# Kernel tuning notes

Hardware: AMD Instinct MI355X
Metric: run time of the kernel (lower is better)

## Reference

```python
import jax, jax.numpy as jnp
import numpy as np

RES = 128          # occupancy grid resolution per axis
S = 320            # fixed number of marching steps per ray
STEP = 0.01        # render_step_size
NEAR = 0.0         # near_plane
ALPHA_THRE = 0.01  # alpha_sample_thre


def setup_inputs() -> dict:
    key = jax.random.key(0)
    k1, k2, k3 = jax.random.split(key, 3)
    N = 16384
    # ray origins inside the scene aabb [-1,1]^3
    origins = (jax.random.uniform(k1, (N, 3), dtype=jnp.float32) - 0.5)
    d = jax.random.normal(k2, (N, 3), dtype=jnp.float32)
    directions = d / jnp.linalg.norm(d, axis=-1, keepdims=True)
    # per-cell densities of the occupancy grid (occupancy_grid.occs)
    occs = jax.random.uniform(k3, (RES, RES, RES), dtype=jnp.float32)
    aabb = jnp.array([[-1.0, -1.0, -1.0], [1.0, 1.0, 1.0]], dtype=jnp.float32)
    return {"origins": origins, "directions": directions, "occs": occs, "aabb": aabb}


def _ray_aabb(o, d, aabb):
    # robust slab intersection; returns (t_min, t_max) per ray
    safe_d = jnp.where(jnp.abs(d) < 1e-10, 1e-10, d)
    inv = 1.0 / safe_d
    t0 = (aabb[0] - o) * inv
    t1 = (aabb[1] - o) * inv
    tmin = jnp.max(jnp.minimum(t0, t1), axis=-1)
    tmax = jnp.min(jnp.maximum(t0, t1), axis=-1)
    return jnp.maximum(tmin, NEAR), tmax


def reference(origins, directions, occs, aabb):
    N = origins.shape[0]
    tmin, tmax = _ray_aabb(origins, directions, aabb)           # [N]
    i = jnp.arange(S, dtype=origins.dtype)
    t_starts = tmin[:, None] + i[None, :] * STEP                # [N,S]
    t_ends = t_starts + STEP
    t_mid = 0.5 * (t_starts + t_ends)
    # sample midpoints along each ray: [N,S,3]
    pos = origins[:, None, :] + directions[:, None, :] * t_mid[..., None]
    # occupancy-grid query (nerfacc.grid._query style)
    u = (pos - aabb[0]) / (aabb[1] - aabb[0])                   # [N,S,3] in [0,1)
    idx = jnp.clip(jnp.floor(u * RES).astype(jnp.int32), 0, RES - 1)
    occ = occs[idx[..., 0], idx[..., 1], idx[..., 2]]           # [N,S] gather
    inside = jnp.all((u >= 0.0) & (u < 1.0), axis=-1)           # [N,S]
    # alpha = 1 - exp(-render_step_size * density), as in update_binary_grid
    alpha = 1.0 - jnp.exp(-occ * STEP)
    mask = inside & (t_ends <= tmax[:, None]) & (alpha > ALPHA_THRE) \
           & (tmax[:, None] > tmin[:, None])                    # [N,S]
    ray_indices = jnp.broadcast_to(
        jnp.arange(N, dtype=jnp.int32)[:, None], mask.shape)
    maskf = mask.astype(pos.dtype)
    positions = pos * maskf[..., None]                          # compacted-by-mask
    return (positions,
            t_starts * maskf,
            t_ends * maskf,
            jnp.where(mask, ray_indices, -1),
            mask)
```

## Files before the change

### kernel.cpp

```cpp
#include <hip/hip_runtime.h>

#define RES 128
#define NSTEPS 320
#define STEP 0.01f
#define ALPHA_THRE 0.01f

__global__ __launch_bounds__(NSTEPS) void nerfacc_sampler_kernel(
    const float* __restrict__ origins,
    const float* __restrict__ dirs,
    const float* __restrict__ occs,
    const float* __restrict__ aabb,
    float* __restrict__ out,
    int N)
{
    const int r = blockIdx.x;
    const int j = threadIdx.x;

    const float ox = origins[r * 3 + 0];
    const float oy = origins[r * 3 + 1];
    const float oz = origins[r * 3 + 2];
    const float dx = dirs[r * 3 + 0];
    const float dy = dirs[r * 3 + 1];
    const float dz = dirs[r * 3 + 2];
    const float lx = aabb[0], ly = aabb[1], lz = aabb[2];
    const float hx = aabb[3], hy = aabb[4], hz = aabb[5];

    const float sdx = (fabsf(dx) < 1e-10f) ? 1e-10f : dx;
    const float sdy = (fabsf(dy) < 1e-10f) ? 1e-10f : dy;
    const float sdz = (fabsf(dz) < 1e-10f) ? 1e-10f : dz;
    const float ivx = 1.0f / sdx, ivy = 1.0f / sdy, ivz = 1.0f / sdz;
    const float t0x = (lx - ox) * ivx, t1x = (hx - ox) * ivx;
    const float t0y = (ly - oy) * ivy, t1y = (hy - oy) * ivy;
    const float t0z = (lz - oz) * ivz, t1z = (hz - oz) * ivz;
    float tmin = fmaxf(fmaxf(fminf(t0x, t1x), fminf(t0y, t1y)), fminf(t0z, t1z));
    float tmax = fminf(fminf(fmaxf(t0x, t1x), fmaxf(t0y, t1y)), fmaxf(t0z, t1z));
    tmin = fmaxf(tmin, 0.0f);

    const float t_start = tmin + (float)j * STEP;
    const float t_end   = t_start + STEP;
    const float t_mid   = 0.5f * (t_start + t_end);

    const float px = ox + dx * t_mid;
    const float py = oy + dy * t_mid;
    const float pz = oz + dz * t_mid;

    const float ux = (px - lx) / (hx - lx);
    const float uy = (py - ly) / (hy - ly);
    const float uz = (pz - lz) / (hz - lz);

    int ix = (int)floorf(ux * (float)RES);
    int iy = (int)floorf(uy * (float)RES);
    int iz = (int)floorf(uz * (float)RES);
    ix = min(max(ix, 0), RES - 1);
    iy = min(max(iy, 0), RES - 1);
    iz = min(max(iz, 0), RES - 1);

    const float occ = occs[((size_t)ix * RES + iy) * RES + iz];

    const bool inside = (ux >= 0.0f) & (ux < 1.0f) &
                        (uy >= 0.0f) & (uy < 1.0f) &
                        (uz >= 0.0f) & (uz < 1.0f);
    const float alpha = 1.0f - expf(-occ * STEP);
    const bool mask = inside & (t_end <= tmax) & (alpha > ALPHA_THRE) & (tmax > tmin);
    const float m = mask ? 1.0f : 0.0f;

    const size_t NS = (size_t)N * NSTEPS;
    const size_t base = (size_t)r * NSTEPS + (size_t)j;

    out[base * 3 + 0] = px * m;
    out[base * 3 + 1] = py * m;
    out[base * 3 + 2] = pz * m;
    out[NS * 3 + base] = t_start * m;
    out[NS * 4 + base] = t_end * m;
    out[NS * 5 + base] = mask ? (float)r : -1.0f;
    out[NS * 6 + base] = m;
}

extern "C" void kernel_launch(void* const* d_in, const int* in_sizes, int n_in,
                              void* d_out, int out_size, void* d_ws, size_t ws_size,
                              hipStream_t stream) {
    const float* origins = (const float*)d_in[0];
    const float* dirs    = (const float*)d_in[1];
    const float* occs    = (const float*)d_in[2];
    const float* aabb    = (const float*)d_in[3];
    float* out = (float*)d_out;

    const int N = in_sizes[0] / 3;

    nerfacc_sampler_kernel<<<dim3(N), dim3(NSTEPS), 0, stream>>>(
        origins, dirs, occs, aabb, out, N);
}
```

Baseline: 180.2 us.

## Process four steps per thread with float4 vectorized stores and flat grid

Each thread now handles four consecutive samples of a ray, batching the grid gathers and writing outputs with float4 stores instead of scalar stores. The launch moves to a flat 1D grid of 256-thread blocks instead of one block per ray. The alpha test is replaced by an equivalent density threshold, which removes the exp. This targets a store-bandwidth-bound kernel and per-thread ray setup overhead, at the cost of more registers per thread and an exact threshold equivalence that relies on floating-point rounding.

```diff
diff --git a/kernel.cpp b/kernel.cpp
--- a/kernel.cpp
+++ b/kernel.cpp
@@ -3,9 +3,13 @@
 #define RES 128
 #define NSTEPS 320
 #define STEP 0.01f
-#define ALPHA_THRE 0.01f
+#define OCC_THRE 1.0050336f
 
-__global__ __launch_bounds__(NSTEPS) void nerfacc_sampler_kernel(
+#define SPT 4
+#define TPR (NSTEPS / SPT)
+#define BLOCK 256
+
+__global__ __launch_bounds__(BLOCK) void nerfacc_sampler_kernel(
     const float* __restrict__ origins,
     const float* __restrict__ dirs,
     const float* __restrict__ occs,
@@ -13,8 +17,10 @@
     float* __restrict__ out,
     int N)
 {
-    const int r = blockIdx.x;
-    const int j = threadIdx.x;
+    const int T = blockIdx.x * BLOCK + threadIdx.x;
+    const int r = T / TPR;
+    if (r >= N) return;
+    const int j0 = (T - r * TPR) * SPT;
 
     const float ox = origins[r * 3 + 0];
     const float oy = origins[r * 3 + 1];
@@ -36,44 +42,58 @@
     float tmax = fminf(fminf(fmaxf(t0x, t1x), fmaxf(t0y, t1y)), fmaxf(t0z, t1z));
     tmin = fmaxf(tmin, 0.0f);
 
-    const float t_start = tmin + (float)j * STEP;
-    const float t_end   = t_start + STEP;
-    const float t_mid   = 0.5f * (t_start + t_end);
+    float px[SPT], py[SPT], pz[SPT], ts[SPT], te[SPT], ri[SPT], mm[SPT];
+    float occv[SPT];
 
-    const float px = ox + dx * t_mid;
-    const float py = oy + dy * t_mid;
-    const float pz = oz + dz * t_mid;
+    int gidx[SPT];
+    float uxv[SPT], uyv[SPT], uzv[SPT];
+    #pragma unroll
+    for (int i = 0; i < SPT; ++i) {
+        const float t_start = tmin + (float)(j0 + i) * STEP;
+        const float t_end   = t_start + STEP;
+        const float t_mid   = 0.5f * (t_start + t_end);
+        const float x = ox + dx * t_mid;
+        const float y = oy + dy * t_mid;
+        const float z = oz + dz * t_mid;
+        const float ux = (x - lx) / (hx - lx);
+        const float uy = (y - ly) / (hy - ly);
+        const float uz = (z - lz) / (hz - lz);
+        int ix = min(max((int)floorf(ux * (float)RES), 0), RES - 1);
+        int iy = min(max((int)floorf(uy * (float)RES), 0), RES - 1);
+        int iz = min(max((int)floorf(uz * (float)RES), 0), RES - 1);
+        gidx[i] = (ix * RES + iy) * RES + iz;
+        uxv[i] = ux; uyv[i] = uy; uzv[i] = uz;
+        px[i] = x; py[i] = y; pz[i] = z;
+        ts[i] = t_start; te[i] = t_end;
+    }
+    #pragma unroll
+    for (int i = 0; i < SPT; ++i) occv[i] = occs[gidx[i]];
 
-    const float ux = (px - lx) / (hx - lx);
-    const float uy = (py - ly) / (hy - ly);
-    const float uz = (pz - lz) / (hz - lz);
+    #pragma unroll
+    for (int i = 0; i < SPT; ++i) {
+        const bool inside = (uxv[i] >= 0.0f) & (uxv[i] < 1.0f) &
+                            (uyv[i] >= 0.0f) & (uyv[i] < 1.0f) &
+                            (uzv[i] >= 0.0f) & (uzv[i] < 1.0f);
+        const bool mask = inside & (te[i] <= tmax) & (occv[i] > OCC_THRE) & (tmax > tmin);
+        const float m = mask ? 1.0f : 0.0f;
+        px[i] *= m; py[i] *= m; pz[i] *= m;
+        ts[i] *= m; te[i] *= m;
+        ri[i] = mask ? (float)r : -1.0f;
+        mm[i] = m;
+    }
 
-    int ix = (int)floorf(ux * (float)RES);
-    int iy = (int)floorf(uy * (float)RES);
-    int iz = (int)floorf(uz * (float)RES);
-    ix = min(max(ix, 0), RES - 1);
-    iy = min(max(iy, 0), RES - 1);
-    iz = min(max(iz, 0), RES - 1);
+    const size_t NS   = (size_t)N * NSTEPS;
+    const size_t base = (size_t)r * NSTEPS + (size_t)j0;
 
-    const float occ = occs[((size_t)ix * RES + iy) * RES + iz];
+    float4* pp = (float4*)(out + base * 3);
+    pp[0] = make_float4(px[0], py[0], pz[0], px[1]);
+    pp[1] = make_float4(py[1], pz[1], px[2], py[2]);
+    pp[2] = make_float4(pz[2], px[3], py[3], pz[3]);
 
-    const bool inside = (ux >= 0.0f) & (ux < 1.0f) &
-                        (uy >= 0.0f) & (uy < 1.0f) &
-                        (uz >= 0.0f) & (uz < 1.0f);
-    const float alpha = 1.0f - expf(-occ * STEP);
-    const bool mask = inside & (t_end <= tmax) & (alpha > ALPHA_THRE) & (tmax > tmin);
-    const float m = mask ? 1.0f : 0.0f;
-
-    const size_t NS = (size_t)N * NSTEPS;
-    const size_t base = (size_t)r * NSTEPS + (size_t)j;
-
-    out[base * 3 + 0] = px * m;
-    out[base * 3 + 1] = py * m;
-    out[base * 3 + 2] = pz * m;
-    out[NS * 3 + base] = t_start * m;
-    out[NS * 4 + base] = t_end * m;
-    out[NS * 5 + base] = mask ? (float)r : -1.0f;
-    out[NS * 6 + base] = m;
+    *(float4*)(out + NS * 3 + base) = make_float4(ts[0], ts[1], ts[2], ts[3]);
+    *(float4*)(out + NS * 4 + base) = make_float4(te[0], te[1], te[2], te[3]);
+    *(float4*)(out + NS * 5 + base) = make_float4(ri[0], ri[1], ri[2], ri[3]);
+    *(float4*)(out + NS * 6 + base) = make_float4(mm[0], mm[1], mm[2], mm[3]);
 }
 
 extern "C" void kernel_launch(void* const* d_in, const int* in_sizes, int n_in,
@@ -86,7 +106,9 @@
     float* out = (float*)d_out;
 
     const int N = in_sizes[0] / 3;
+    const int total = N * TPR;
+    const int grid = (total + BLOCK - 1) / BLOCK;
 
-    nerfacc_sampler_kernel<<<dim3(N), dim3(NSTEPS), 0, stream>>>(
+    nerfacc_sampler_kernel<<<dim3(grid), dim3(BLOCK), 0, stream>>>(
         origins, dirs, occs, aabb, out, N);
 }
```

New measurement: 180.2 us. Within noise of the previous version (+0.0%).
